# Optimization experiments

Hardware: AMD Instinct MI355X
Metric: run time of the kernel (lower is better)

## Reference

```python
import jax, jax.numpy as jnp
import numpy as np
import math

B, S, E = 4, 2048, 1024

def setup_inputs() -> dict:
    key = jax.random.key(0)
    ks = jax.random.split(key, 12)
    scale = 1.0 / math.sqrt(E)
    inp = {
        "query": jax.random.normal(ks[0], (B, S, E), jnp.float32),
        "key_": jax.random.normal(ks[1], (B, S, E), jnp.float32),
        "value": jax.random.normal(ks[2], (B, S, E), jnp.float32),
        # causal mask, broadcast over batch: 1 = keep, 0 = mask
        "mask": jnp.broadcast_to(jnp.tril(jnp.ones((S, S), jnp.int32)), (B, S, S)),
        "Wq": jax.random.uniform(ks[3], (E, E), jnp.float32, -scale, scale),
        "bq": jax.random.uniform(ks[4], (E,), jnp.float32, -scale, scale),
        "Wk": jax.random.uniform(ks[5], (E, E), jnp.float32, -scale, scale),
        "bk": jax.random.uniform(ks[6], (E,), jnp.float32, -scale, scale),
        "Wv": jax.random.uniform(ks[7], (E, E), jnp.float32, -scale, scale),
        "bv": jax.random.uniform(ks[8], (E,), jnp.float32, -scale, scale),
        "Wo": jax.random.uniform(ks[9], (E, E), jnp.float32, -scale, scale),
        "bo": jax.random.uniform(ks[10], (E,), jnp.float32, -scale, scale),
    }
    return inp

def reference(query, key_, value, mask, Wq, bq, Wk, bk, Wv, bv, Wo, bo):
    # Linear projections (torch Linear: x @ W.T + b)
    Q = jnp.einsum('bse,fe->bsf', query, Wq) + bq
    K = jnp.einsum('bse,fe->bsf', key_, Wk) + bk
    V = jnp.einsum('bse,fe->bsf', value, Wv) + bv
    # NOTE: module never splits heads; scores over full embed_dim, scaled by sqrt(embed_dim)
    scores = jnp.einsum('bqe,bke->bqk', Q, K) / jnp.sqrt(jnp.asarray(E, Q.dtype))
    scores = jnp.where(mask == 0, -jnp.inf, scores)
    attn = jax.nn.softmax(scores, axis=-1)
    attn_out = jnp.einsum('bqk,bke->bqe', attn, V)
    return jnp.einsum('bse,fe->bsf', attn_out, Wo) + bo
```

## Files before the change

### kernel.cpp

```cpp
#include <hip/hip_runtime.h>

typedef __bf16 bf16;
typedef __attribute__((ext_vector_type(8))) __bf16 bf16x8;
typedef __attribute__((ext_vector_type(4))) __bf16 bf16x4;
typedef __attribute__((ext_vector_type(2))) __bf16 bf16x2;
typedef __attribute__((ext_vector_type(4))) float f32x4;

#define DEVINL __device__ __forceinline__

DEVINL void gload_lds16(const bf16* g, bf16* l) {
    __builtin_amdgcn_global_load_lds(
        (__attribute__((address_space(1))) unsigned int*)(unsigned long long)g,
        (__attribute__((address_space(3))) unsigned int*)l,
        16, 0, 0);
}

DEVINL void xcd_swizzle(int& bx, int& by) {
    const int gx = gridDim.x, gy = gridDim.y;
    const int l = blockIdx.y * gx + blockIdx.x;
    const int xcd = l & 7;
    const int li = l >> 3;
    by = xcd * (gy >> 3) + li / gx;
    bx = li - (li / gx) * gx;
}

DEVINL void xcd_swizzle_bal(int& bx, int& by) {
    const int gx = gridDim.x, gy = gridDim.y;
    const int l = blockIdx.y * gx + blockIdx.x;
    const int xcd = l & 7;
    const int li = l >> 3;
    const int j = li / gx;
    bx = li - j * gx;
    by = j ? (gy - 1 - xcd) : xcd;
}

__global__ __launch_bounds__(256) void cvt3_f32_to_bf16(
    const float* __restrict__ a, const float* __restrict__ b,
    const float* __restrict__ c, bf16* __restrict__ out, int n4) {
    int i = blockIdx.x * blockDim.x + threadIdx.x;
    if (i >= n4) return;
    const float* src = (blockIdx.z == 0) ? a : (blockIdx.z == 1) ? b : c;
    bf16* dst = out + (size_t)blockIdx.z * (size_t)n4 * 4;
    float4 f = ((const float4*)src)[i];
    bf16x4 o;
    o.x = (bf16)f.x; o.y = (bf16)f.y; o.z = (bf16)f.z; o.w = (bf16)f.w;
    ((bf16x4*)dst)[i] = o;
}

__global__ __launch_bounds__(256) void cvt4_f32_to_bf16(
    const float* __restrict__ a, const float* __restrict__ b,
    const float* __restrict__ c, const float* __restrict__ d,
    bf16* __restrict__ out, int n4) {
    int i = blockIdx.x * blockDim.x + threadIdx.x;
    if (i >= n4) return;
    const float* src = (blockIdx.z == 0) ? a : (blockIdx.z == 1) ? b
                     : (blockIdx.z == 2) ? c : d;
    bf16* dst = out + (size_t)blockIdx.z * (size_t)n4 * 4;
    float4 f = ((const float4*)src)[i];
    bf16x4 o;
    o.x = (bf16)f.x; o.y = (bf16)f.y; o.z = (bf16)f.z; o.w = (bf16)f.w;
    ((bf16x4*)dst)[i] = o;
}

__global__ __launch_bounds__(256) void transpose_bf16(
    const unsigned short* __restrict__ in, unsigned short* __restrict__ out,
    int R, int C) {
    __shared__ unsigned short t[64][65];
    const size_t bo = (size_t)blockIdx.z * R * C;
    const int r0 = blockIdx.y * 64, c0 = blockIdx.x * 64;
#pragma unroll
    for (int i = 0; i < 16; i++) {
        int lin = threadIdx.x + i * 256;
        int r = lin >> 6, c = lin & 63;
        t[r][c] = in[bo + (size_t)(r0 + r) * C + (c0 + c)];
    }
    __syncthreads();
#pragma unroll
    for (int i = 0; i < 16; i++) {
        int lin = threadIdx.x + i * 256;
        int r = lin >> 6, c = lin & 63;
        out[bo + (size_t)(c0 + r) * R + (r0 + c)] = t[c][r];
    }
}

__global__ __launch_bounds__(256) void bias_fold(
    const float* __restrict__ Wo, const float* __restrict__ bv,
    const float* __restrict__ bo, float* __restrict__ bout) {
    const int e = blockIdx.x * 4 + (threadIdx.x >> 6);
    const int lane = threadIdx.x & 63;
    float s = 0.f;
    for (int k = lane; k < 1024; k += 64) s += Wo[e * 1024 + k] * bv[k];
#pragma unroll
    for (int off = 32; off > 0; off >>= 1) s += __shfl_xor(s, off, 64);
    if (lane == 0) bout[e] = s + bo[e];
}

template <int EPI>
__global__ __launch_bounds__(256) void gemm_bt128(
    const bf16* __restrict__ A, const bf16* __restrict__ B,
    const float* __restrict__ bias0, const float* __restrict__ bias1,
    const float* __restrict__ bias2, void* __restrict__ Cv,
    int M, int N, int K,
    long long sA, long long sB, long long sC,
    float scale) {
    int bx, by;
    xcd_swizzle(bx, by);
    const int bz = blockIdx.z;
    const int m0 = by * 128, n0 = bx * 128;

    A += (size_t)bz * sA;
    B += (size_t)bz * sB;
    const float* bias = (bz == 0) ? bias0 : (bz == 1) ? bias1 : bias2;

    __shared__ __align__(16) bf16 As[2][128 * 32];
    __shared__ __align__(16) bf16 Bs[2][128 * 32];

    const int tid = threadIdx.x;
    const int wave = tid >> 6;
    const int lane = tid & 63;
    const int lr = lane & 15;
    const int lq = lane >> 4;
    const int wm = (wave >> 1) * 64;
    const int wn = (wave & 1) * 64;
    const int srow = lane >> 2;
    const int scol = ((lane & 3) ^ ((lane >> 3) & 3)) * 8;

    const bf16* gA = A + (size_t)(m0 + wave * 16 + srow) * K + scol;
    const bf16* gB = B + (size_t)(n0 + wave * 16 + srow) * K + scol;
    const size_t rowskip = (size_t)64 * K;
    const int rsw = (lq ^ ((lr >> 1) & 3)) * 8;

    f32x4 acc[4][4];
    const f32x4 fzero = {0.f, 0.f, 0.f, 0.f};
#pragma unroll
    for (int i = 0; i < 4; i++)
#pragma unroll
        for (int j = 0; j < 4; j++) acc[i][j] = fzero;

#define STAGE128(bufi)                                          \
    do {                                                        \
        gload_lds16(gA,           As[bufi] + wave * 512);       \
        gload_lds16(gA + rowskip, As[bufi] + (wave + 4) * 512); \
        gload_lds16(gB,           Bs[bufi] + wave * 512);       \
        gload_lds16(gB + rowskip, Bs[bufi] + (wave + 4) * 512); \
        gA += 32; gB += 32;                                     \
    } while (0)

    STAGE128(0);
    int cur = 0;
    for (int k0 = 0; k0 < K; k0 += 32) {
        __syncthreads();
        if (k0 + 32 < K) STAGE128(cur ^ 1);

        bf16x8 af[4], bfr[4];
#pragma unroll
        for (int i = 0; i < 4; i++)
            af[i] = *(const bf16x8*)(As[cur] + (wm + i * 16 + lr) * 32 + rsw);
#pragma unroll
        for (int j = 0; j < 4; j++)
            bfr[j] = *(const bf16x8*)(Bs[cur] + (wn + j * 16 + lr) * 32 + rsw);
#pragma unroll
        for (int i = 0; i < 4; i++)
#pragma unroll
            for (int j = 0; j < 4; j++)
                acc[i][j] = __builtin_amdgcn_mfma_f32_16x16x32_bf16(
                    af[i], bfr[j], acc[i][j], 0, 0, 0);
        cur ^= 1;
    }
#undef STAGE128

#pragma unroll
    for (int j = 0; j < 4; j++) {
        const int col = n0 + wn + j * 16 + lr;
        const float bb = bias ? bias[col] : 0.0f;
#pragma unroll
        for (int i = 0; i < 4; i++) {
            const int rowb = m0 + wm + i * 16 + lq * 4;
#pragma unroll
            for (int r = 0; r < 4; r++) {
                if (EPI == 0)
                    ((bf16*)Cv)[(size_t)bz * sC + (size_t)(rowb + r) * N + col] =
                        (bf16)(acc[i][j][r] * scale + bb);
                else
                    ((float*)Cv)[(size_t)bz * sC + (size_t)(rowb + r) * N + col] =
                        acc[i][j][r] * scale + bb;
            }
        }
    }
}

template <int EPI>
__global__ __launch_bounds__(512) void gemm_pipe(
    const bf16* __restrict__ A, const bf16* __restrict__ B,
    const float* __restrict__ bias0, const float* __restrict__ bias1,
    const float* __restrict__ bias2, void* __restrict__ Cv,
    int M, int N, int K,
    long long sA, long long sB, long long sC,
    float scale, int causal) {
    int bx, by;
    if (causal) xcd_swizzle_bal(bx, by);
    else        xcd_swizzle(bx, by);
    const int bz = blockIdx.z;
    const int m0 = by * 128, n0 = bx * 256;
    if (causal == 1 && n0 > m0 + 127) return;
    int Keff = K;
    if (causal == 2) { Keff = m0 + 128; if (Keff > K) Keff = K; }
    const int NT = Keff >> 5;

    A += (size_t)bz * sA;
    B += (size_t)bz * sB;
    const float* bias = (bz == 0) ? bias0 : (bz == 1) ? bias1 : bias2;

    __shared__ __align__(16) bf16 As[4][128 * 32];
    __shared__ __align__(16) bf16 Bs[4][256 * 32];

    const int tid = threadIdx.x;
    const int wave = tid >> 6;
    const int lane = tid & 63;
    const int lr = lane & 15;
    const int lq = lane >> 4;
    const int wm = (wave >> 2) * 64;
    const int wn = (wave & 3) * 64;

    const int srow = lane >> 2;
    const int scol = ((lane & 3) ^ ((lane >> 3) & 3)) * 8;
    const bf16* gA  = A + (size_t)(m0 + wave * 16 + srow) * K + scol;
    const bf16* gB0 = B + (size_t)(n0 + wave * 32 + srow) * K + scol;
    const size_t rowskip = (size_t)16 * K;

    const int rsw = (lq ^ ((lr >> 1) & 3)) * 8;

    f32x4 acc[4][4];
    const f32x4 fzero = {0.f, 0.f, 0.f, 0.f};
#pragma unroll
    for (int i = 0; i < 4; i++)
#pragma unroll
        for (int j = 0; j < 4; j++) acc[i][j] = fzero;

#define STAGEP(bufi, koff)                                               \
    do {                                                                 \
        gload_lds16(gA + (koff),            As[bufi] + wave * 512);      \
        gload_lds16(gB0 + (koff),           Bs[bufi] + wave * 1024);     \
        gload_lds16(gB0 + rowskip + (koff), Bs[bufi] + wave * 1024 + 512); \
    } while (0)

    if (NT > 0) STAGEP(0, 0);
    if (NT > 1) STAGEP(1, 32);
    if (NT > 2) STAGEP(2, 64);
    if (NT > 2)      asm volatile("s_waitcnt vmcnt(6)" ::: "memory");
    else if (NT > 1) asm volatile("s_waitcnt vmcnt(3)" ::: "memory");
    else             asm volatile("s_waitcnt vmcnt(0)" ::: "memory");
    __builtin_amdgcn_s_barrier();

    for (int t = 0; t < NT; ++t) {
        const int bfi = t & 3;

        bf16x8 af[4], bfr[4];
#pragma unroll
        for (int i = 0; i < 4; i++)
            af[i] = *(const bf16x8*)(As[bfi] + (wm + i * 16 + lr) * 32 + rsw);
#pragma unroll
        for (int j = 0; j < 4; j++)
            bfr[j] = *(const bf16x8*)(Bs[bfi] + (wn + j * 16 + lr) * 32 + rsw);

        if (t + 3 < NT) STAGEP((t + 3) & 3, (t + 3) * 32);

        if (t + 3 < NT)      asm volatile("s_waitcnt vmcnt(6)" ::: "memory");
        else if (t + 2 < NT) asm volatile("s_waitcnt vmcnt(3)" ::: "memory");
        else                 asm volatile("s_waitcnt vmcnt(0)" ::: "memory");
        __builtin_amdgcn_s_barrier();

        __builtin_amdgcn_s_setprio(1);
#pragma unroll
        for (int i = 0; i < 4; i++)
#pragma unroll
            for (int j = 0; j < 4; j++)
                acc[i][j] = __builtin_amdgcn_mfma_f32_16x16x32_bf16(
                    af[i], bfr[j], acc[i][j], 0, 0, 0);
        __builtin_amdgcn_s_setprio(0);
        __builtin_amdgcn_s_barrier();
    }
#undef STAGEP

#pragma unroll
    for (int j = 0; j < 4; j++) {
        const int col = n0 + wn + j * 16 + lr;
        const float bb = bias ? bias[col] : 0.0f;
#pragma unroll
        for (int i = 0; i < 4; i++) {
            const int rowb = m0 + wm + i * 16 + lq * 4;
#pragma unroll
            for (int r = 0; r < 4; r++) {
                if (EPI == 0)
                    ((bf16*)Cv)[(size_t)bz * sC + (size_t)(rowb + r) * N + col] =
                        (bf16)(acc[i][j][r] * scale + bb);
                else
                    ((float*)Cv)[(size_t)bz * sC + (size_t)(rowb + r) * N + col] =
                        acc[i][j][r] * scale + bb;
            }
        }
    }
}

__global__ __launch_bounds__(256) void softmax_causal(
    const bf16* __restrict__ Sc, bf16* __restrict__ P, int S) {
    const int row = blockIdx.x;
    const int q = row & (S - 1);
    const bf16* src = Sc + (size_t)row * S;
    bf16* dst = P + (size_t)row * S;
    const int L = q + 1;
    const int tid = threadIdx.x;

    float v[8];
    float mx = -3.0e38f;
#pragma unroll
    for (int i = 0; i < 4; i++) {
        int k = (i * 256 + tid) * 2;
        bf16x2 u = ((const bf16x2*)src)[i * 256 + tid];
        v[2 * i]     = (k < L)     ? (float)u.x : -3.0e38f;
        v[2 * i + 1] = (k + 1 < L) ? (float)u.y : -3.0e38f;
        mx = fmaxf(mx, fmaxf(v[2 * i], v[2 * i + 1]));
    }
#pragma unroll
    for (int off = 32; off > 0; off >>= 1) mx = fmaxf(mx, __shfl_xor(mx, off, 64));
    __shared__ float redm[4], reds[4];
    if ((tid & 63) == 0) redm[tid >> 6] = mx;
    __syncthreads();
    mx = fmaxf(fmaxf(redm[0], redm[1]), fmaxf(redm[2], redm[3]));

    float sum = 0.f;
#pragma unroll
    for (int i = 0; i < 8; i++) {
        float e = (v[i] > -1.0e38f) ? __expf(v[i] - mx) : 0.f;
        v[i] = e;
        sum += e;
    }
#pragma unroll
    for (int off = 32; off > 0; off >>= 1) sum += __shfl_xor(sum, off, 64);
    if ((tid & 63) == 0) reds[tid >> 6] = sum;
    __syncthreads();
    sum = reds[0] + reds[1] + reds[2] + reds[3];
    const float inv = 1.0f / sum;
#pragma unroll
    for (int i = 0; i < 4; i++) {
        bf16x2 o;
        o.x = (bf16)(v[2 * i] * inv);
        o.y = (bf16)(v[2 * i + 1] * inv);
        ((bf16x2*)dst)[i * 256 + tid] = o;
    }
}

extern "C" void kernel_launch(void* const* d_in, const int* in_sizes, int n_in,
                              void* d_out, int out_size, void* d_ws, size_t ws_size,
                              hipStream_t stream) {
    const int B = 4, S = 2048, E = 1024;
    const size_t SBE = (size_t)B * S * E;
    const size_t EE = (size_t)E * E;

    const float* q_in = (const float*)d_in[0];
    const float* k_in = (const float*)d_in[1];
    const float* v_in = (const float*)d_in[2];
    const float* Wq = (const float*)d_in[4];
    const float* bq = (const float*)d_in[5];
    const float* Wk = (const float*)d_in[6];
    const float* bk = (const float*)d_in[7];
    const float* Wv = (const float*)d_in[8];
    const float* bv = (const float*)d_in[9];
    const float* Wo = (const float*)d_in[10];
    const float* bo = (const float*)d_in[11];

    char* ws = (char*)d_ws;
    bf16* qkvb = (bf16*)ws;
    bf16* Sc = (bf16*)ws;
    bf16* WvT = (bf16*)(ws + 3 * SBE * 2);
    float* bout = (float*)(ws + 3 * SBE * 2 + EE * 2);
    char* p = ws + (size_t)B * S * S * 4;
    bf16* QKVb = (bf16*)p; p += 3 * SBE * 2;
    bf16* VWt = (bf16*)p; p += SBE * 2;
    bf16* Pb = (bf16*)p; p += (size_t)B * S * S * 2;
    bf16* Wb = (bf16*)p; p += 4 * EE * 2;

    bf16* Qb = QKVb;
    bf16* Kb = QKVb + SBE;
    bf16* VW = QKVb + 2 * SBE;
    bf16* Wob = Wb + 3 * EE;
    bf16* Wvo = Wb + 2 * EE;

    dim3 blk(256), blk512(512);

    dim3 gcvt3((int)(SBE / 4 / 256), 1, 3);
    cvt3_f32_to_bf16<<<gcvt3, blk, 0, stream>>>(q_in, k_in, v_in, qkvb, (int)(SBE / 4));
    dim3 gcvt4((int)(EE / 4 / 256), 1, 4);
    cvt4_f32_to_bf16<<<gcvt4, blk, 0, stream>>>(Wq, Wk, Wv, Wo, Wb, (int)(EE / 4));

    dim3 gtw(16, 16, 1);
    transpose_bf16<<<gtw, blk, 0, stream>>>((const unsigned short*)(Wb + 2 * EE),
                                            (unsigned short*)WvT, E, E);
    dim3 gwvo(E / 128, E / 128, 1);
    gemm_bt128<0><<<gwvo, blk, 0, stream>>>(Wob, WvT, nullptr, nullptr, nullptr,
                                            Wvo, E, E, E, 0, 0, 0, 1.f);
    bias_fold<<<256, blk, 0, stream>>>(Wo, bv, bo, bout);

    dim3 gproj(E / 256, (B * S) / 128, 3);
    gemm_pipe<0><<<gproj, blk512, 0, stream>>>(qkvb, Wb, bq, bk, nullptr, QKVb,
                                               B * S, E, E,
                                               (long long)SBE, (long long)EE,
                                               (long long)SBE, 1.f, 0);

    dim3 gt(E / 64, S / 64, B);
    transpose_bf16<<<gt, blk, 0, stream>>>((const unsigned short*)VW,
                                           (unsigned short*)VWt, S, E);

    dim3 gsc(S / 256, S / 128, B);
    gemm_pipe<0><<<gsc, blk512, 0, stream>>>(Qb, Kb, nullptr, nullptr, nullptr, Sc,
                                             S, S, E,
                                             (long long)S * E, (long long)S * E,
                                             (long long)S * S, 0.03125f, 1);

    softmax_causal<<<B * S, blk, 0, stream>>>(Sc, Pb, S);

    dim3 gpv(E / 256, S / 128, B);
    gemm_pipe<1><<<gpv, blk512, 0, stream>>>(Pb, VWt, bout, bout, bout,
                                             (float*)d_out, S, E, S,
                                             (long long)S * S, (long long)E * S,
                                             (long long)S * E, 1.f, 0);
}
```

Baseline: 398.7 us.

## Use 256x256 GEMM tiles, single-barrier pipeline, and causal-trimmed PV kernel

```diff
diff --git a/kernel.cpp b/kernel.cpp
--- a/kernel.cpp
+++ b/kernel.cpp
@@ -190,7 +190,7 @@
 }
 
 template <int EPI>
-__global__ __launch_bounds__(512) void gemm_pipe(
+__global__ __launch_bounds__(512, 2) void gemm_pipe256(
     const bf16* __restrict__ A, const bf16* __restrict__ B,
     const float* __restrict__ bias0, const float* __restrict__ bias1,
     const float* __restrict__ bias2, void* __restrict__ Cv,
@@ -198,20 +198,17 @@
     long long sA, long long sB, long long sC,
     float scale, int causal) {
     int bx, by;
-    if (causal) xcd_swizzle_bal(bx, by);
-    else        xcd_swizzle(bx, by);
+    xcd_swizzle(bx, by);
     const int bz = blockIdx.z;
-    const int m0 = by * 128, n0 = bx * 256;
-    if (causal == 1 && n0 > m0 + 127) return;
-    int Keff = K;
-    if (causal == 2) { Keff = m0 + 128; if (Keff > K) Keff = K; }
-    const int NT = Keff >> 5;
+    const int m0 = by * 256, n0 = bx * 256;
+    if (causal == 1 && n0 > m0 + 255) return;
+    const int NT = K >> 5;
 
     A += (size_t)bz * sA;
     B += (size_t)bz * sB;
     const float* bias = (bz == 0) ? bias0 : (bz == 1) ? bias1 : bias2;
 
-    __shared__ __align__(16) bf16 As[4][128 * 32];
+    __shared__ __align__(16) bf16 As[4][256 * 32];
     __shared__ __align__(16) bf16 Bs[4][256 * 32];
 
     const int tid = threadIdx.x;
@@ -219,66 +216,63 @@
     const int lane = tid & 63;
     const int lr = lane & 15;
     const int lq = lane >> 4;
-    const int wm = (wave >> 2) * 64;
+    const int wm = (wave >> 2) * 128;
     const int wn = (wave & 3) * 64;
 
     const int srow = lane >> 2;
     const int scol = ((lane & 3) ^ ((lane >> 3) & 3)) * 8;
-    const bf16* gA  = A + (size_t)(m0 + wave * 16 + srow) * K + scol;
-    const bf16* gB0 = B + (size_t)(n0 + wave * 32 + srow) * K + scol;
-    const size_t rowskip = (size_t)16 * K;
+    const bf16* gA = A + (size_t)(m0 + wave * 16 + srow) * K + scol;
+    const bf16* gB = B + (size_t)(n0 + wave * 16 + srow) * K + scol;
+    const size_t rowskip = (size_t)128 * K;
 
     const int rsw = (lq ^ ((lr >> 1) & 3)) * 8;
 
-    f32x4 acc[4][4];
+    f32x4 acc[8][4];
     const f32x4 fzero = {0.f, 0.f, 0.f, 0.f};
 #pragma unroll
-    for (int i = 0; i < 4; i++)
+    for (int i = 0; i < 8; i++)
 #pragma unroll
         for (int j = 0; j < 4; j++) acc[i][j] = fzero;
 
-#define STAGEP(bufi, koff)                                               \
-    do {                                                                 \
-        gload_lds16(gA + (koff),            As[bufi] + wave * 512);      \
-        gload_lds16(gB0 + (koff),           Bs[bufi] + wave * 1024);     \
-        gload_lds16(gB0 + rowskip + (koff), Bs[bufi] + wave * 1024 + 512); \
+#define STAGEP(bufi, koff)                                                 \
+    do {                                                                   \
+        gload_lds16(gA + (koff),           As[bufi] + wave * 512);         \
+        gload_lds16(gA + rowskip + (koff), As[bufi] + (wave + 8) * 512);   \
+        gload_lds16(gB + (koff),           Bs[bufi] + wave * 512);         \
+        gload_lds16(gB + rowskip + (koff), Bs[bufi] + (wave + 8) * 512);   \
     } while (0)
 
     if (NT > 0) STAGEP(0, 0);
     if (NT > 1) STAGEP(1, 32);
     if (NT > 2) STAGEP(2, 64);
-    if (NT > 2)      asm volatile("s_waitcnt vmcnt(6)" ::: "memory");
-    else if (NT > 1) asm volatile("s_waitcnt vmcnt(3)" ::: "memory");
-    else             asm volatile("s_waitcnt vmcnt(0)" ::: "memory");
-    __builtin_amdgcn_s_barrier();
 
     for (int t = 0; t < NT; ++t) {
+        const int nf = NT - t;
+        if (nf > 2)       asm volatile("s_waitcnt vmcnt(8)" ::: "memory");
+        else if (nf == 2) asm volatile("s_waitcnt vmcnt(4)" ::: "memory");
+        else              asm volatile("s_waitcnt vmcnt(0)" ::: "memory");
+        __builtin_amdgcn_s_barrier();
+        asm volatile("" ::: "memory");
+
+        if (t + 3 < NT) STAGEP((t + 3) & 3, (t + 3) * 32);
+
         const int bfi = t & 3;
-
-        bf16x8 af[4], bfr[4];
-#pragma unroll
-        for (int i = 0; i < 4; i++)
+        bf16x8 af[8], bfr[4];
+#pragma unroll
+        for (int i = 0; i < 8; i++)
             af[i] = *(const bf16x8*)(As[bfi] + (wm + i * 16 + lr) * 32 + rsw);
 #pragma unroll
         for (int j = 0; j < 4; j++)
             bfr[j] = *(const bf16x8*)(Bs[bfi] + (wn + j * 16 + lr) * 32 + rsw);
 
-        if (t + 3 < NT) STAGEP((t + 3) & 3, (t + 3) * 32);
-
-        if (t + 3 < NT)      asm volatile("s_waitcnt vmcnt(6)" ::: "memory");
-        else if (t + 2 < NT) asm volatile("s_waitcnt vmcnt(3)" ::: "memory");
-        else                 asm volatile("s_waitcnt vmcnt(0)" ::: "memory");
-        __builtin_amdgcn_s_barrier();
-
         __builtin_amdgcn_s_setprio(1);
 #pragma unroll
-        for (int i = 0; i < 4; i++)
+        for (int i = 0; i < 8; i++)
 #pragma unroll
             for (int j = 0; j < 4; j++)
                 acc[i][j] = __builtin_amdgcn_mfma_f32_16x16x32_bf16(
                     af[i], bfr[j], acc[i][j], 0, 0, 0);
         __builtin_amdgcn_s_setprio(0);
-        __builtin_amdgcn_s_barrier();
     }
 #undef STAGEP
 
@@ -287,7 +281,7 @@
         const int col = n0 + wn + j * 16 + lr;
         const float bb = bias ? bias[col] : 0.0f;
 #pragma unroll
-        for (int i = 0; i < 4; i++) {
+        for (int i = 0; i < 8; i++) {
             const int rowb = m0 + wm + i * 16 + lq * 4;
 #pragma unroll
             for (int r = 0; r < 4; r++) {
@@ -298,6 +292,105 @@
                     ((float*)Cv)[(size_t)bz * sC + (size_t)(rowb + r) * N + col] =
                         acc[i][j][r] * scale + bb;
             }
+        }
+    }
+}
+
+__global__ __launch_bounds__(256, 2) void gemm_pv128(
+    const bf16* __restrict__ A, const bf16* __restrict__ B,
+    const float* __restrict__ bias, float* __restrict__ C,
+    int M, int N, int K,
+    long long sA, long long sB, long long sC,
+    float scale) {
+    int bx, by;
+    xcd_swizzle_bal(bx, by);
+    const int bz = blockIdx.z;
+    const int m0 = by * 128, n0 = bx * 128;
+    int Keff = m0 + 128; if (Keff > K) Keff = K;
+    const int NT = Keff >> 5;
+
+    A += (size_t)bz * sA;
+    B += (size_t)bz * sB;
+
+    __shared__ __align__(16) bf16 As[4][128 * 32];
+    __shared__ __align__(16) bf16 Bs[4][128 * 32];
+
+    const int tid = threadIdx.x;
+    const int wave = tid >> 6;
+    const int lane = tid & 63;
+    const int lr = lane & 15;
+    const int lq = lane >> 4;
+    const int wm = (wave >> 1) * 64;
+    const int wn = (wave & 1) * 64;
+
+    const int srow = lane >> 2;
+    const int scol = ((lane & 3) ^ ((lane >> 3) & 3)) * 8;
+    const bf16* gA = A + (size_t)(m0 + wave * 16 + srow) * K + scol;
+    const bf16* gB = B + (size_t)(n0 + wave * 16 + srow) * K + scol;
+    const size_t rowskip = (size_t)64 * K;
+
+    const int rsw = (lq ^ ((lr >> 1) & 3)) * 8;
+
+    f32x4 acc[4][4];
+    const f32x4 fzero = {0.f, 0.f, 0.f, 0.f};
+#pragma unroll
+    for (int i = 0; i < 4; i++)
+#pragma unroll
+        for (int j = 0; j < 4; j++) acc[i][j] = fzero;
+
+#define STAGEV(bufi, koff)                                                 \
+    do {                                                                   \
+        gload_lds16(gA + (koff),           As[bufi] + wave * 512);         \
+        gload_lds16(gA + rowskip + (koff), As[bufi] + (wave + 4) * 512);   \
+        gload_lds16(gB + (koff),           Bs[bufi] + wave * 512);         \
+        gload_lds16(gB + rowskip + (koff), Bs[bufi] + (wave + 4) * 512);   \
+    } while (0)
+
+    if (NT > 0) STAGEV(0, 0);
+    if (NT > 1) STAGEV(1, 32);
+    if (NT > 2) STAGEV(2, 64);
+
+    for (int t = 0; t < NT; ++t) {
+        const int nf = NT - t;
+        if (nf > 2)       asm volatile("s_waitcnt vmcnt(8)" ::: "memory");
+        else if (nf == 2) asm volatile("s_waitcnt vmcnt(4)" ::: "memory");
+        else              asm volatile("s_waitcnt vmcnt(0)" ::: "memory");
+        __builtin_amdgcn_s_barrier();
+        asm volatile("" ::: "memory");
+
+        if (t + 3 < NT) STAGEV((t + 3) & 3, (t + 3) * 32);
+
+        const int bfi = t & 3;
+        bf16x8 af[4], bfr[4];
+#pragma unroll
+        for (int i = 0; i < 4; i++)
+            af[i] = *(const bf16x8*)(As[bfi] + (wm + i * 16 + lr) * 32 + rsw);
+#pragma unroll
+        for (int j = 0; j < 4; j++)
+            bfr[j] = *(const bf16x8*)(Bs[bfi] + (wn + j * 16 + lr) * 32 + rsw);
+
+        __builtin_amdgcn_s_setprio(1);
+#pragma unroll
+        for (int i = 0; i < 4; i++)
+#pragma unroll
+            for (int j = 0; j < 4; j++)
+                acc[i][j] = __builtin_amdgcn_mfma_f32_16x16x32_bf16(
+                    af[i], bfr[j], acc[i][j], 0, 0, 0);
+        __builtin_amdgcn_s_setprio(0);
+    }
+#undef STAGEV
+
+#pragma unroll
+    for (int j = 0; j < 4; j++) {
+        const int col = n0 + wn + j * 16 + lr;
+        const float bb = bias[col];
+#pragma unroll
+        for (int i = 0; i < 4; i++) {
+            const int rowb = m0 + wm + i * 16 + lq * 4;
+#pragma unroll
+            for (int r = 0; r < 4; r++)
+                C[(size_t)bz * sC + (size_t)(rowb + r) * N + col] =
+                    acc[i][j][r] * scale + bb;
         }
     }
 }
@@ -401,27 +494,26 @@
                                             Wvo, E, E, E, 0, 0, 0, 1.f);
     bias_fold<<<256, blk, 0, stream>>>(Wo, bv, bo, bout);
 
-    dim3 gproj(E / 256, (B * S) / 128, 3);
-    gemm_pipe<0><<<gproj, blk512, 0, stream>>>(qkvb, Wb, bq, bk, nullptr, QKVb,
-                                               B * S, E, E,
-                                               (long long)SBE, (long long)EE,
-                                               (long long)SBE, 1.f, 0);
+    dim3 gproj(E / 256, (B * S) / 256, 3);
+    gemm_pipe256<0><<<gproj, blk512, 0, stream>>>(qkvb, Wb, bq, bk, nullptr, QKVb,
+                                                  B * S, E, E,
+                                                  (long long)SBE, (long long)EE,
+                                                  (long long)SBE, 1.f, 0);
 
     dim3 gt(E / 64, S / 64, B);
     transpose_bf16<<<gt, blk, 0, stream>>>((const unsigned short*)VW,
                                            (unsigned short*)VWt, S, E);
 
-    dim3 gsc(S / 256, S / 128, B);
-    gemm_pipe<0><<<gsc, blk512, 0, stream>>>(Qb, Kb, nullptr, nullptr, nullptr, Sc,
-                                             S, S, E,
-                                             (long long)S * E, (long long)S * E,
-                                             (long long)S * S, 0.03125f, 1);
+    dim3 gsc(S / 256, S / 256, B);
+    gemm_pipe256<0><<<gsc, blk512, 0, stream>>>(Qb, Kb, nullptr, nullptr, nullptr, Sc,
+                                                S, S, E,
+                                                (long long)S * E, (long long)S * E,
+                                                (long long)S * S, 0.03125f, 1);
 
     softmax_causal<<<B * S, blk, 0, stream>>>(Sc, Pb, S);
 
-    dim3 gpv(E / 256, S / 128, B);
-    gemm_pipe<1><<<gpv, blk512, 0, stream>>>(Pb, VWt, bout, bout, bout,
-                                             (float*)d_out, S, E, S,
-                                             (long long)S * S, (long long)E * S,
-                                             (long long)S * E, 1.f, 0);
-}
+    dim3 gpv(E / 128, S / 128, B);
+    gemm_pv128<<<gpv, blk, 0, stream>>>(Pb, VWt, bout, (float*)d_out, S, E, S,
+                                        (long long)S * S, (long long)E * S,
+                                        (long long)S * E, 1.f);
+}
```

After: 427.3 us. +7.2%, slower.
